# Kernel optimization log

Hardware: AMD Instinct MI355X
Metric: run time of the kernel (lower is better)

The kernel has to match this reference:

```python
import jax, jax.numpy as jnp
import numpy as np

# dims
L, E, D, DFF, H = 4, 4, 512, 2048, 8
B, T, S, K = 16, 256, 512, 2
HD = D // H


def _ln(x, g, b, eps=1e-5):
    m = x.mean(-1, keepdims=True)
    v = ((x - m) ** 2).mean(-1, keepdims=True)
    return (x - m) / jnp.sqrt(v + eps) * g + b


def _mha(xq, xkv, in_w, in_b, out_w, out_b):
    # torch nn.MultiheadAttention (batch_first), no masks, eval mode
    qw, kw, vw = jnp.split(in_w, 3, axis=0)
    qb, kb, vb = jnp.split(in_b, 3)
    q = xq @ qw.T + qb                       # [B,T,D]
    k = xkv @ kw.T + kb                      # [B,S,D]
    v = xkv @ vw.T + vb
    def heads(t):
        b, s, _ = t.shape
        return t.reshape(b, s, H, HD).transpose(0, 2, 1, 3)
    q, k, v = heads(q), heads(k), heads(v)   # [B,H,*,HD]
    scale = 1.0 / float(np.sqrt(HD))
    a = jax.nn.softmax(jnp.einsum('bhtd,bhsd->bhts', q, k) * scale, axis=-1)
    o = jnp.einsum('bhts,bhsd->bhtd', a, v)
    o = o.transpose(0, 2, 1, 3).reshape(xq.shape[0], xq.shape[1], D)
    return o @ out_w.T + out_b


def _expert(p, x, mem):
    (siw, sib, sow, sob, ciw, cib, cow, cob,
     l1w, l1b, l2w, l2b, g1, b1, g2, b2, g3, b3) = p
    sa = _mha(x, x, siw, sib, sow, sob)
    x = _ln(x + sa, g1, b1)
    ca = _mha(x, mem, ciw, cib, cow, cob)
    x = _ln(x + ca, g2, b2)
    ffn = jax.nn.relu(x @ l1w.T + l1b) @ l2w.T + l2b
    x = _ln(x + ffn, g3, b3)
    return x


def _forward(tgt, memory, router_w, params):
    x = tgt
    for l in range(L):
        pooled = x.mean(axis=1)                      # [B,D] sample-level routing
        logits = pooled @ router_w[l].T              # [B,E]
        vals, idx = jax.lax.top_k(logits, K)
        w = jax.nn.softmax(vals.astype(jnp.float32), axis=-1).astype(x.dtype)
        # dense [B,E] combine weights: zero for unselected experts -> same math
        wf = jnp.zeros((x.shape[0], E), x.dtype).at[jnp.arange(x.shape[0])[:, None], idx].add(w)
        p_l = jax.tree_util.tree_map(lambda a: a[l], params)   # each [E,...]
        outs = jax.vmap(_expert, in_axes=(0, None, None))(p_l, x, memory)  # [E,B,T,D]
        x = jnp.einsum('be,ebtd->btd', wf, outs)
    return x


def setup_inputs() -> dict:
    key = jax.random.key(0)
    ks = jax.random.split(key, 16)
    n = lambda k, shape: jax.random.normal(k, shape, jnp.float32) * 0.02
    return {
        'tgt': jax.random.normal(ks[0], (B, T, D), jnp.float32),
        'memory': jax.random.normal(ks[1], (B, S, D), jnp.float32),
        'router_w': n(ks[2], (L, E, D)),
        'sa_in_w': n(ks[3], (L, E, 3 * D, D)), 'sa_in_b': jnp.zeros((L, E, 3 * D)),
        'sa_out_w': n(ks[4], (L, E, D, D)), 'sa_out_b': jnp.zeros((L, E, D)),
        'ca_in_w': n(ks[5], (L, E, 3 * D, D)), 'ca_in_b': jnp.zeros((L, E, 3 * D)),
        'ca_out_w': n(ks[6], (L, E, D, D)), 'ca_out_b': jnp.zeros((L, E, D)),
        'lin1_w': n(ks[7], (L, E, DFF, D)), 'lin1_b': jnp.zeros((L, E, DFF)),
        'lin2_w': n(ks[8], (L, E, D, DFF)), 'lin2_b': jnp.zeros((L, E, D)),
        'n1_g': jnp.ones((L, E, D)), 'n1_b': jnp.zeros((L, E, D)),
        'n2_g': jnp.ones((L, E, D)), 'n2_b': jnp.zeros((L, E, D)),
        'n3_g': jnp.ones((L, E, D)), 'n3_b': jnp.zeros((L, E, D)),
    }


def reference(tgt, memory, router_w, sa_in_w, sa_in_b, sa_out_w, sa_out_b,
              ca_in_w, ca_in_b, ca_out_w, ca_out_b, lin1_w, lin1_b, lin2_w, lin2_b,
              n1_g, n1_b, n2_g, n2_b, n3_g, n3_b):
    params = (sa_in_w, sa_in_b, sa_out_w, sa_out_b, ca_in_w, ca_in_b, ca_out_w, ca_out_b,
              lin1_w, lin1_b, lin2_w, lin2_b, n1_g, n1_b, n2_g, n2_b, n3_g, n3_b)
    return _forward(tgt, memory, router_w, params)
```

## Files before the change

### kernel.cpp

```cpp
#include <hip/hip_runtime.h>
#include <hip/hip_bf16.h>

#define L_ 4
#define E_ 4
#define D_ 512
#define DFF_ 2048
#define H_ 8
#define B_ 16
#define T_ 256
#define S_ 512
#define HD_ 64
#define NSLOT 32

typedef __attribute__((ext_vector_type(4))) float f32x4;
typedef __attribute__((ext_vector_type(8))) short bf16x8;
typedef __attribute__((ext_vector_type(4))) int i32x4;

static __device__ __forceinline__ float bf2f(unsigned short u){
  union{float f; unsigned u;} c; c.u = ((unsigned)u)<<16; return c.f;
}
static __device__ __forceinline__ unsigned short f2bf(float f){
  union{float f; unsigned u;} c; c.f=f;
  unsigned u=c.u;
  return (unsigned short)((u + 0x7FFFu + ((u>>16)&1u))>>16);
}

static __device__ __forceinline__ void gload16(const unsigned short* g, unsigned short* l){
  __builtin_amdgcn_global_load_lds(
      (const __attribute__((address_space(1))) void*)g,
      (__attribute__((address_space(3))) void*)l, 16, 0, 0);
}

static __device__ __forceinline__ int xcd_swz(int orig, int nwg){
  int q = nwg >> 3, r = nwg & 7;
  int xcd = orig & 7, idx = orig >> 3;
  return (xcd < r) ? (xcd*(q+1) + idx) : (r*(q+1) + (xcd-r)*q + idx);
}

__global__ void __launch_bounds__(256) route_k(const float* __restrict__ x,
    const float* __restrict__ rw, int* __restrict__ eidx, float* __restrict__ wgt)
{
  __shared__ float pooled[D_];
  __shared__ float logit[E_];
  int b = blockIdx.x, tid = threadIdx.x;
  for (int d = tid; d < D_; d += 256) {
    float s = 0.f;
    const float* xp = x + ((long)b*T_)*D_ + d;
    for (int t=0;t<T_;t++) s += xp[(long)t*D_];
    pooled[d] = s * (1.f/T_);
  }
  __syncthreads();
  int wave = tid>>6, lane = tid&63;
  {
    float s=0.f;
    const float* w = rw + (long)wave*D_;
    for (int d=lane; d<D_; d+=64) s += pooled[d]*w[d];
    #pragma unroll
    for (int o=32;o;o>>=1) s += __shfl_xor(s,o);
    if (lane==0) logit[wave] = s;
  }
  __syncthreads();
  if (tid==0){
    int i1=0; float v1=logit[0];
    for (int e=1;e<E_;e++) if (logit[e] > v1){ v1=logit[e]; i1=e; }
    int i2=-1; float v2=-3.4e38f;
    for (int e=0;e<E_;e++) if (e!=i1 && logit[e] > v2){ v2=logit[e]; i2=e; }
    float e2 = __expf(v2 - v1);
    float w1 = 1.f/(1.f+e2);
    eidx[2*b]=i1; eidx[2*b+1]=i2;
    wgt[2*b]=w1; wgt[2*b+1]=e2*w1;
  }
}

__global__ void __launch_bounds__(256) cast_bf16_k(const float* __restrict__ in,
    unsigned short* __restrict__ out, long n){
  long i = ((long)blockIdx.x*blockDim.x + threadIdx.x)*4;
  long st = (long)gridDim.x*blockDim.x*4;
  for (; i<n; i+=st){
    float4 v = *(const float4*)(in+i);
    ushort4 o; o.x=f2bf(v.x); o.y=f2bf(v.y); o.z=f2bf(v.z); o.w=f2bf(v.w);
    *(ushort4*)(out+i) = o;
  }
}

__global__ void __launch_bounds__(256) cast_weights_k(
    const float* __restrict__ s0, const float* __restrict__ s1,
    const float* __restrict__ s2, const float* __restrict__ s3,
    const float* __restrict__ s4, const float* __restrict__ s5,
    unsigned short* __restrict__ d0, unsigned short* __restrict__ d1,
    unsigned short* __restrict__ d2, unsigned short* __restrict__ d3,
    unsigned short* __restrict__ d4, unsigned short* __restrict__ d5)
{
  const long N0=(long)E_*3*D_*D_, N1=(long)E_*D_*D_;
  const long N2=N0, N3=N1, N4=(long)E_*DFF_*D_, N5=N4;
  const long total = N0+N1+N2+N3+N4+N5;
  long i = ((long)blockIdx.x*256 + threadIdx.x)*4;
  long st = (long)gridDim.x*256*4;
  for (; i<total; i+=st){
    const float* s; unsigned short* d; long j = i;
    if (j < N0){ s=s0; d=d0; }
    else if ((j-=N0) < N1){ s=s1; d=d1; }
    else if ((j-=N1) < N2){ s=s2; d=d2; }
    else if ((j-=N2) < N3){ s=s3; d=d3; }
    else if ((j-=N3) < N4){ s=s4; d=d4; }
    else { j-=N4; s=s5; d=d5; }
    float4 v = *(const float4*)(s+j);
    ushort4 o; o.x=f2bf(v.x); o.y=f2bf(v.y); o.z=f2bf(v.z); o.w=f2bf(v.w);
    *(ushort4*)(d+j) = o;
  }
}

__global__ void __launch_bounds__(256) vtrans_k(const unsigned short* __restrict__ src,
    long sSlot, int ld, unsigned short* __restrict__ dst, int rows)
{
  __shared__ unsigned short t[64][68];
  int s0 = blockIdx.x*64; int h = blockIdx.y; int slot = blockIdx.z;
  const unsigned short* sp = src + (long)slot*sSlot + (long)h*64;
  int c = threadIdx.x&63, w = threadIdx.x>>6;
  #pragma unroll
  for (int i=0;i<16;i++){
    int r = i*4 + w;
    t[r][c] = sp[(long)(s0+r)*ld + c];
  }
  __syncthreads();
  unsigned short* dp = dst + ((long)slot*H_ + h)*((long)64*rows) + s0;
  #pragma unroll
  for (int i=0;i<16;i++){
    int d = i*4 + w;
    dp[(long)d*rows + c] = t[c][d];
  }
}

template<int NT>
__global__ void __launch_bounds__(256) fattn_k(
    const unsigned short* __restrict__ Qg, long qSlot, int ldq,
    const unsigned short* __restrict__ Kg, long kSlot, int ldk,
    const unsigned short* __restrict__ Vtg,
    unsigned short* __restrict__ Og, long oSlot, int ldo)
{
  constexpr int SLEN = NT*64;
  __shared__ unsigned short K_lds[64][72];
  __shared__ unsigned short V_lds[64][72];
  __shared__ unsigned short P_lds[4][16][72];

  int nwg = gridDim.x*gridDim.y;
  int wg = xcd_swz(blockIdx.x + gridDim.x*blockIdx.y, nwg);
  int qb = wg % gridDim.x;
  int z  = wg / gridDim.x;
  int slot = z >> 3, h = z & 7;
  int tid = threadIdx.x, wave = tid>>6, lane = tid&63;
  int lr = lane&15, lg = lane>>4;
  int lk = lg*8;

  const unsigned short* Qp = Qg + (long)slot*qSlot + (long)h*HD_;
  const unsigned short* Kp = Kg + (long)slot*kSlot + (long)h*HD_;
  const unsigned short* Vp = Vtg + (long)z*((long)HD_*SLEN);

  bf16x8 qf[2];
  {
    int qrow = qb*64 + wave*16 + lr;
    const unsigned short* qr = Qp + (long)qrow*ldq;
    qf[0] = *(const bf16x8*)(qr + lk);
    qf[1] = *(const bf16x8*)(qr + 32 + lk);
  }

  float m_prev[4], l_run[4];
  f32x4 acc_o[4];
  #pragma unroll
  for (int r=0;r<4;r++){ m_prev[r]=-1e30f; l_run[r]=0.f; }
  #pragma unroll
  for (int ni=0;ni<4;ni++) acc_o[ni]=(f32x4){0.f,0.f,0.f,0.f};

  int srow = tid>>3, sch = tid&7;

  i32x4 kr0 = *(const i32x4*)(Kp + (long)srow*ldk + sch*8);
  i32x4 kr1 = *(const i32x4*)(Kp + (long)(srow+32)*ldk + sch*8);
  i32x4 vr0 = *(const i32x4*)(Vp + (long)srow*SLEN + sch*8);
  i32x4 vr1 = *(const i32x4*)(Vp + (long)(srow+32)*SLEN + sch*8);

  for (int t=0; t<NT; ++t){
    __syncthreads();
    *(i32x4*)&K_lds[srow][sch*8] = kr0;
    *(i32x4*)&K_lds[srow+32][sch*8] = kr1;
    *(i32x4*)&V_lds[srow][sch*8] = vr0;
    *(i32x4*)&V_lds[srow+32][sch*8] = vr1;
    __syncthreads();

    int tn = (t+1 < NT) ? t+1 : t;
    int k0n = tn*64;
    kr0 = *(const i32x4*)(Kp + (long)(k0n+srow)*ldk + sch*8);
    kr1 = *(const i32x4*)(Kp + (long)(k0n+srow+32)*ldk + sch*8);
    vr0 = *(const i32x4*)(Vp + (long)srow*SLEN + k0n + sch*8);
    vr1 = *(const i32x4*)(Vp + (long)(srow+32)*SLEN + k0n + sch*8);

    f32x4 s[4];
    #pragma unroll
    for (int ni=0;ni<4;ni++) s[ni]=(f32x4){0.f,0.f,0.f,0.f};
    __builtin_amdgcn_s_setprio(1);
    #pragma unroll
    for (int ki=0;ki<2;ki++){
      #pragma unroll
      for (int ni=0;ni<4;ni++){
        bf16x8 kf = *(const bf16x8*)&K_lds[ni*16+lr][ki*32+lk];
        s[ni] = __builtin_amdgcn_mfma_f32_16x16x32_bf16(qf[ki], kf, s[ni],0,0,0);
      }
    }
    __builtin_amdgcn_s_setprio(0);
    float tmax[4], corr[4], mnew[4];
    #pragma unroll
    for (int r=0;r<4;r++){
      tmax[r] = fmaxf(fmaxf(s[0][r],s[1][r]),fmaxf(s[2][r],s[3][r]));
      #pragma unroll
      for (int msk=1; msk<16; msk<<=1) tmax[r]=fmaxf(tmax[r], __shfl_xor(tmax[r],msk));
      mnew[r] = fmaxf(m_prev[r], tmax[r]);
      corr[r] = __expf(m_prev[r]-mnew[r]);
      m_prev[r] = mnew[r];
    }
    float rs[4] = {0.f,0.f,0.f,0.f};
    #pragma unroll
    for (int ni=0;ni<4;ni++){
      #pragma unroll
      for (int r=0;r<4;r++){
        float p = __expf(s[ni][r]-mnew[r]);
        rs[r] += p;
        P_lds[wave][lg*4+r][ni*16+lr] = f2bf(p);
      }
    }
    #pragma unroll
    for (int r=0;r<4;r++){
      #pragma unroll
      for (int msk=1; msk<16; msk<<=1) rs[r] += __shfl_xor(rs[r],msk);
      l_run[r] = l_run[r]*corr[r] + rs[r];
      #pragma unroll
      for (int ni=0;ni<4;ni++) acc_o[ni][r] *= corr[r];
    }
    __builtin_amdgcn_s_setprio(1);
    #pragma unroll
    for (int ki=0;ki<2;ki++){
      bf16x8 pf = *(const bf16x8*)&P_lds[wave][lr][ki*32+lk];
      #pragma unroll
      for (int ni=0;ni<4;ni++){
        bf16x8 vf = *(const bf16x8*)&V_lds[ni*16+lr][ki*32+lk];
        acc_o[ni] = __builtin_amdgcn_mfma_f32_16x16x32_bf16(pf, vf, acc_o[ni],0,0,0);
      }
    }
    __builtin_amdgcn_s_setprio(0);
  }
  unsigned short* Op = Og + (long)slot*oSlot + (long)h*HD_;
  #pragma unroll
  for (int r=0;r<4;r++){
    float inv = 1.f/l_run[r];
    int q = qb*64 + wave*16 + lg*4 + r;
    #pragma unroll
    for (int ni=0;ni<4;ni++)
      Op[(long)q*ldo + ni*16 + lr] = f2bf(acc_o[ni][r]*inv);
  }
}

template<int BM, int BN, int WTM, int WTN, int BK>
__global__ void __launch_bounds__(512) gemm_lds(
    const unsigned short* __restrict__ A, long aSlot, int aDiv, long aHead, int lda,
    const unsigned short* __restrict__ W, long wSlot, long wHead, long wExp, int ldw,
    const int* __restrict__ eidx, const float* __restrict__ bias, long biasExp,
    void* __restrict__ Cp, long cSlot, long cHead, int ldc,
    int K, int HZ, int f32out, int relu, int scaleNlim, float scaleVal)
{
  constexpr int WAVES_N = BN/WTN;
  constexpr int MI = WTM/16, NI = WTN/16;
  constexpr int SLOTS = BK/8;
  static_assert((BM/WTM)*(BN/WTN) == 8, "8 waves");
  static_assert((BM*SLOTS)%512==0 && (BN*SLOTS)%512==0, "stage coverage");
  __shared__ unsigned short smem[2*(BM+BN)*BK];

  int nwg = gridDim.x*gridDim.y*gridDim.z;
  int wg = xcd_swz(blockIdx.x + gridDim.x*(blockIdx.y + gridDim.y*blockIdx.z), nwg);
  int bx = wg % gridDim.x; int t1 = wg / gridDim.x;
  int by = t1 % gridDim.y; int z  = t1 / gridDim.y;

  int slot = z / HZ;
  int h = z - slot*HZ;
  int e = eidx ? eidx[slot] : 0;
  const unsigned short* Ap = A + (long)(slot/aDiv)*aSlot + (long)h*aHead;
  const unsigned short* Wp = W + (long)slot*wSlot + (long)h*wHead + (long)e*wExp;
  const float* bp = bias ? (bias + (long)e*biasExp) : nullptr;

  int tid  = threadIdx.x;
  int wave = tid>>6, lane = tid&63;
  int wm = wave / WAVES_N, wn = wave % WAVES_N;
  int bm0 = by*BM;
  int bn0 = bx*BN;
  int lr = lane&15;
  int lg = lane>>4;
  int swz = (BK==64) ? (lr&7) : ((lr>>1)&3);

  Ap += (long)bm0*lda;
  Wp += (long)bn0*ldw;

  f32x4 acc[MI][NI];
  #pragma unroll
  for (int i=0;i<MI;i++)
  #pragma unroll
  for (int j=0;j<NI;j++) acc[i][j] = (f32x4){0.f,0.f,0.f,0.f};

  auto stage = [&](int buf, int k0){
    unsigned short* as = &smem[(size_t)buf*(BM+BN)*BK];
    unsigned short* bs = as + BM*BK;
    #pragma unroll
    for (int i=0;i<BM*SLOTS/512;i++){
      int cch = i*512 + tid;
      int row = cch / SLOTS, c = cch % SLOTS;
      int cs = (BK==64) ? (c ^ (row&7)) : (c ^ ((row>>1)&3));
      gload16(Ap + (long)row*lda + k0 + (cs<<3), as + cch*8);
    }
    #pragma unroll
    for (int i=0;i<BN*SLOTS/512;i++){
      int cch = i*512 + tid;
      int row = cch / SLOTS, c = cch % SLOTS;
      int cs = (BK==64) ? (c ^ (row&7)) : (c ^ ((row>>1)&3));
      gload16(Wp + (long)row*ldw + k0 + (cs<<3), bs + cch*8);
    }
  };

  auto compute = [&](int buf){
    unsigned short* as = &smem[(size_t)buf*(BM+BN)*BK];
    unsigned short* bs = as + BM*BK;
    #pragma unroll
    for (int ki=0;ki<BK/32;ki++){
      bf16x8 af[MI], bfr[NI];
      #pragma unroll
      for (int mi=0;mi<MI;mi++){
        int row = wm*WTM + mi*16 + lr;
        af[mi] = *(const bf16x8*)&as[row*BK + (((ki*4+lg) ^ swz)<<3)];
      }
      #pragma unroll
      for (int ni=0;ni<NI;ni++){
        int row = wn*WTN + ni*16 + lr;
        bfr[ni] = *(const bf16x8*)&bs[row*BK + (((ki*4+lg) ^ swz)<<3)];
      }
      __builtin_amdgcn_s_setprio(1);
      #pragma unroll
      for (int mi=0;mi<MI;mi++)
      #pragma unroll
      for (int ni=0;ni<NI;ni++)
        acc[mi][ni] = __builtin_amdgcn_mfma_f32_16x16x32_bf16(af[mi], bfr[ni], acc[mi][ni], 0,0,0);
      __builtin_amdgcn_s_setprio(0);
    }
  };

  int NT = K / BK;
  stage(0, 0);
  __syncthreads();
  int cur = 0;
  for (int t=0; t<NT; ++t){
    if (t+1 < NT) stage(cur^1, (t+1)*BK);
    compute(cur);
    __syncthreads();
    cur ^= 1;
  }

  long cbase = (long)slot*cSlot + (long)h*cHead;
  int rbase = lg*4;
  #pragma unroll
  for (int mi=0;mi<MI;mi++)
  #pragma unroll
  for (int ni=0;ni<NI;ni++){
    f32x4 v = acc[mi][ni];
    int n = bn0 + wn*WTN + ni*16 + lr;
    float bv = bp ? bp[n] : 0.f;
    float scv = (n < scaleNlim) ? scaleVal : 1.f;
    #pragma unroll
    for (int r=0;r<4;r++){
      int m = bm0 + wm*WTM + mi*16 + rbase + r;
      float val = (v[r] + bv) * scv;
      if (relu) val = fmaxf(val, 0.f);
      long o = cbase + (long)m*ldc + n;
      if (f32out) ((float*)Cp)[o] = val;
      else ((unsigned short*)Cp)[o] = f2bf(val);
    }
  }
}

__global__ void __launch_bounds__(256) add_ln_k(
    const float* __restrict__ Ab, int aDiv, long aStride,
    const float* __restrict__ Bb, long bStride,
    const float* __restrict__ G, const float* __restrict__ Bt,
    const int* __restrict__ eidx,
    float* __restrict__ OutF, unsigned short* __restrict__ OutB)
{
  int row = blockIdx.x*4 + (threadIdx.x>>6);
  int slot = row>>8, t = row&255;
  int lane = threadIdx.x&63;
  const float* a = Ab + (long)(slot/aDiv)*aStride + (long)t*D_;
  const float* b = Bb + (long)slot*bStride + (long)t*D_;
  int e = eidx[slot];
  const float* g  = G  + (long)e*D_;
  const float* bt = Bt + (long)e*D_;
  float x[8]; float s=0.f;
  #pragma unroll
  for (int i=0;i<8;i++){ x[i] = a[lane+i*64]+b[lane+i*64]; s+=x[i]; }
  #pragma unroll
  for (int o=32;o;o>>=1) s += __shfl_xor(s,o);
  float m = s*(1.f/D_);
  float q=0.f;
  #pragma unroll
  for (int i=0;i<8;i++){ float d=x[i]-m; q+=d*d; }
  #pragma unroll
  for (int o=32;o;o>>=1) q += __shfl_xor(q,o);
  float rs = rsqrtf(q*(1.f/D_)+1e-5f);
  long ob = (long)slot*(T_*D_) + (long)t*D_;
  #pragma unroll
  for (int i=0;i<8;i++){
    int d = lane+i*64;
    float y = (x[i]-m)*rs*g[d]+bt[d];
    OutF[ob+d]=y;
    if (OutB) OutB[ob+d]=f2bf(y);
  }
}

__global__ void __launch_bounds__(256) add_ln_comb_k(
    const float* __restrict__ x2, const float* __restrict__ proj,
    const float* __restrict__ G, const float* __restrict__ Bt,
    const int* __restrict__ eidx, const float* __restrict__ wgt,
    float* __restrict__ dstF, unsigned short* __restrict__ dstB)
{
  int row = blockIdx.x*4 + (threadIdx.x>>6);
  int b = row>>8, t = row&255;
  int lane = threadIdx.x&63;
  float out[8];
  #pragma unroll
  for (int i=0;i<8;i++) out[i]=0.f;
  #pragma unroll
  for (int s2i=0;s2i<2;s2i++){
    int slot = 2*b + s2i;
    int e = eidx[slot];
    float w = wgt[slot];
    const float* a = x2 + (long)slot*(T_*D_) + (long)t*D_;
    const float* p = proj + (long)slot*(T_*D_) + (long)t*D_;
    const float* g  = G  + (long)e*D_;
    const float* bt = Bt + (long)e*D_;
    float x[8]; float s=0.f;
    #pragma unroll
    for (int i=0;i<8;i++){ x[i] = a[lane+i*64]+p[lane+i*64]; s+=x[i]; }
    #pragma unroll
    for (int o=32;o;o>>=1) s += __shfl_xor(s,o);
    float m = s*(1.f/D_);
    float q=0.f;
    #pragma unroll
    for (int i=0;i<8;i++){ float d=x[i]-m; q+=d*d; }
    #pragma unroll
    for (int o=32;o;o>>=1) q += __shfl_xor(q,o);
    float rs = rsqrtf(q*(1.f/D_)+1e-5f);
    #pragma unroll
    for (int i=0;i<8;i++){
      int d = lane+i*64;
      out[i] += w*((x[i]-m)*rs*g[d]+bt[d]);
    }
  }
  long ob = (long)row*D_;
  #pragma unroll
  for (int i=0;i<8;i++){
    int d = lane+i*64;
    dstF[ob+d] = out[i];
    dstB[ob+d] = f2bf(out[i]);
  }
}

extern "C" void kernel_launch(void* const* d_in, const int* in_sizes, int n_in,
                              void* d_out, int out_size, void* d_ws, size_t ws_size,
                              hipStream_t stream)
{
  const float* tgt      = (const float*)d_in[0];
  const float* memory   = (const float*)d_in[1];
  const float* router_w = (const float*)d_in[2];
  const float* sa_in_w  = (const float*)d_in[3];
  const float* sa_in_b  = (const float*)d_in[4];
  const float* sa_out_w = (const float*)d_in[5];
  const float* sa_out_b = (const float*)d_in[6];
  const float* ca_in_w  = (const float*)d_in[7];
  const float* ca_in_b  = (const float*)d_in[8];
  const float* ca_out_w = (const float*)d_in[9];
  const float* ca_out_b = (const float*)d_in[10];
  const float* lin1_w   = (const float*)d_in[11];
  const float* lin1_b   = (const float*)d_in[12];
  const float* lin2_w   = (const float*)d_in[13];
  const float* lin2_b   = (const float*)d_in[14];
  const float* n1_g = (const float*)d_in[15];
  const float* n1_b = (const float*)d_in[16];
  const float* n2_g = (const float*)d_in[17];
  const float* n2_b = (const float*)d_in[18];
  const float* n3_g = (const float*)d_in[19];
  const float* n3_b = (const float*)d_in[20];

  char* ws = (char*)d_ws;
  size_t off = 0;
  auto alloc = [&](size_t bytes)->char*{
    char* p = ws + off; off += (bytes + 255) & ~(size_t)255; return p;
  };
  unsigned short* xb    = (unsigned short*)alloc(2ull*B_*T_*D_);
  unsigned short* memb  = (unsigned short*)alloc(2ull*B_*S_*D_);
  float*          x     = (float*)alloc(4ull*B_*T_*D_);
  int*            eidx  = (int*)alloc(4ull*NSLOT);
  float*          wgt   = (float*)alloc(4ull*NSLOT);
  unsigned short* wSaIn  = (unsigned short*)alloc(2ull*E_*3*D_*D_);
  unsigned short* wSaOut = (unsigned short*)alloc(2ull*E_*D_*D_);
  unsigned short* wCaIn  = (unsigned short*)alloc(2ull*E_*3*D_*D_);
  unsigned short* wCaOut = (unsigned short*)alloc(2ull*E_*D_*D_);
  unsigned short* wL1    = (unsigned short*)alloc(2ull*E_*DFF_*D_);
  unsigned short* wL2    = (unsigned short*)alloc(2ull*E_*D_*DFF_);
  unsigned short* qkv   = (unsigned short*)alloc(2ull*NSLOT*T_*3*D_);
  unsigned short* ffh   = (unsigned short*)alloc(2ull*NSLOT*T_*DFF_);
  unsigned short* attn  = (unsigned short*)alloc(2ull*NSLOT*T_*D_);
  float*          proj  = (float*)alloc(4ull*NSLOT*T_*D_);
  float*          x1    = (float*)alloc(4ull*NSLOT*T_*D_);
  unsigned short* x1b   = (unsigned short*)alloc(2ull*NSLOT*T_*D_);
  unsigned short* cq    = (unsigned short*)alloc(2ull*NSLOT*T_*D_);
  unsigned short* mkv   = (unsigned short*)alloc(2ull*NSLOT*S_*2*D_);
  float*          x2    = (float*)alloc(4ull*NSLOT*T_*D_);
  unsigned short* x2b   = (unsigned short*)alloc(2ull*NSLOT*T_*D_);
  unsigned short* Vt1   = cq;
  unsigned short* Vt2   = qkv;

  cast_bf16_k<<<1024,256,0,stream>>>(tgt,    xb,   (long)B_*T_*D_);
  cast_bf16_k<<<1024,256,0,stream>>>(memory, memb, (long)B_*S_*D_);

  const float* xcur = tgt;
  for (int l=0; l<L_; ++l){
    route_k<<<B_,256,0,stream>>>(xcur, router_w + (size_t)l*E_*D_, eidx, wgt);
    cast_weights_k<<<2048,256,0,stream>>>(
      sa_in_w  + (size_t)l*E_*3*D_*D_, sa_out_w + (size_t)l*E_*D_*D_,
      ca_in_w  + (size_t)l*E_*3*D_*D_, ca_out_w + (size_t)l*E_*D_*D_,
      lin1_w   + (size_t)l*E_*DFF_*D_, lin2_w   + (size_t)l*E_*D_*DFF_,
      wSaIn, wSaOut, wCaIn, wCaOut, wL1, wL2);

    gemm_lds<128,256,64,64,32><<<dim3(6,2,NSLOT),512,0,stream>>>(
      xb, (long)T_*D_, 2, 0, D_,
      wSaIn, 0, 0, (long)3*D_*D_, D_,
      eidx, sa_in_b + (size_t)l*E_*3*D_, 3*D_,
      qkv, (long)T_*3*D_, 0, 3*D_,
      512, 1, 0, 0, D_, 0.125f);
    vtrans_k<<<dim3(T_/64,H_,NSLOT),256,0,stream>>>(
      qkv + 2*D_, (long)T_*3*D_, 3*D_, Vt1, T_);
    fattn_k<4><<<dim3(T_/64, NSLOT*H_),256,0,stream>>>(
      qkv, (long)T_*3*D_, 3*D_,
      qkv + D_, (long)T_*3*D_, 3*D_,
      Vt1, attn, (long)T_*D_, D_);
    gemm_lds<128,128,64,32,64><<<dim3(4,2,NSLOT),512,0,stream>>>(
      attn, (long)T_*D_, 1, 0, D_,
      wSaOut, 0, 0, (long)D_*D_, D_,
      eidx, sa_out_b + (size_t)l*E_*D_, D_,
      proj, (long)T_*D_, 0, D_,
      512, 1, 1, 0, 0, 1.f);
    add_ln_k<<<2048,256,0,stream>>>(xcur, 2, (long)T_*D_, proj, (long)T_*D_,
      n1_g + (size_t)l*E_*D_, n1_b + (size_t)l*E_*D_, eidx, x1, x1b);
    gemm_lds<128,128,64,32,64><<<dim3(4,2,NSLOT),512,0,stream>>>(
      x1b, (long)T_*D_, 1, 0, D_,
      wCaIn, 0, 0, (long)3*D_*D_, D_,
      eidx, ca_in_b + (size_t)l*E_*3*D_, 3*D_,
      cq, (long)T_*D_, 0, D_,
      512, 1, 0, 0, D_, 0.125f);
    gemm_lds<128,256,64,64,32><<<dim3(4,4,NSLOT),512,0,stream>>>(
      memb, (long)S_*D_, 2, 0, D_,
      wCaIn + (size_t)D_*D_, 0, 0, (long)3*D_*D_, D_,
      eidx, ca_in_b + (size_t)l*E_*3*D_ + D_, 3*D_,
      mkv, (long)S_*2*D_, 0, 2*D_,
      512, 1, 0, 0, 0, 1.f);
    vtrans_k<<<dim3(S_/64,H_,NSLOT),256,0,stream>>>(
      mkv + D_, (long)S_*2*D_, 2*D_, Vt2, S_);
    fattn_k<8><<<dim3(T_/64, NSLOT*H_),256,0,stream>>>(
      cq, (long)T_*D_, D_,
      mkv, (long)S_*2*D_, 2*D_,
      Vt2, attn, (long)T_*D_, D_);
    gemm_lds<128,128,64,32,64><<<dim3(4,2,NSLOT),512,0,stream>>>(
      attn, (long)T_*D_, 1, 0, D_,
      wCaOut, 0, 0, (long)D_*D_, D_,
      eidx, ca_out_b + (size_t)l*E_*D_, D_,
      proj, (long)T_*D_, 0, D_,
      512, 1, 1, 0, 0, 1.f);
    add_ln_k<<<2048,256,0,stream>>>(x1, 1, (long)T_*D_, proj, (long)T_*D_,
      n2_g + (size_t)l*E_*D_, n2_b + (size_t)l*E_*D_, eidx, x2, x2b);
    gemm_lds<128,256,64,64,32><<<dim3(8,2,NSLOT),512,0,stream>>>(
      x2b, (long)T_*D_, 1, 0, D_,
      wL1, 0, 0, (long)DFF_*D_, D_,
      eidx, lin1_b + (size_t)l*E_*DFF_, DFF_,
      ffh, (long)T_*DFF_, 0, DFF_,
      512, 1, 0, 1, 0, 1.f);
    gemm_lds<128,128,64,32,64><<<dim3(4,2,NSLOT),512,0,stream>>>(
      ffh, (long)T_*DFF_, 1, 0, DFF_,
      wL2, 0, 0, (long)D_*DFF_, DFF_,
      eidx, lin2_b + (size_t)l*E_*D_, D_,
      proj, (long)T_*D_, 0, D_,
      2048, 1, 1, 0, 0, 1.f);
    float* dstF = (l==L_-1) ? (float*)d_out : x;
    add_ln_comb_k<<<1024,256,0,stream>>>(x2, proj,
      n3_g + (size_t)l*E_*D_, n3_b + (size_t)l*E_*D_, eidx, wgt, dstF, xb);
    xcur = x;
  }
}
```

Measured before the change: 1.093 ms.

## Split-K the D-output GEMMs into two partials and skip redundant softmax rescaling

The three GEMMs that produce D-wide fp32 outputs (self-attn out, cross-attn out, FFN lin2) are split along K into two halves. Each half writes to a separate buffer (proj, proj2), and the following add+LayerNorm kernels sum the two partials, so grids with few workgroups get twice as many. The flash-attention loop also skips the running-max correction (an exp plus rescaling of the accumulators) when no row max increases in the wave. The cost is an extra fp32 partial buffer write and read per GEMM, plus a divergent branch.

```diff
diff --git a/kernel.cpp b/kernel.cpp
--- a/kernel.cpp
+++ b/kernel.cpp
@@ -206,22 +206,31 @@
       }
     }
     __builtin_amdgcn_s_setprio(0);
-    float tmax[4], corr[4], mnew[4];
+    float tmax[4];
     #pragma unroll
     for (int r=0;r<4;r++){
       tmax[r] = fmaxf(fmaxf(s[0][r],s[1][r]),fmaxf(s[2][r],s[3][r]));
       #pragma unroll
       for (int msk=1; msk<16; msk<<=1) tmax[r]=fmaxf(tmax[r], __shfl_xor(tmax[r],msk));
-      mnew[r] = fmaxf(m_prev[r], tmax[r]);
-      corr[r] = __expf(m_prev[r]-mnew[r]);
-      m_prev[r] = mnew[r];
+    }
+    bool inc = (tmax[0]>m_prev[0])|(tmax[1]>m_prev[1])|(tmax[2]>m_prev[2])|(tmax[3]>m_prev[3]);
+    if (__any(inc)){
+      #pragma unroll
+      for (int r=0;r<4;r++){
+        float mnew = fmaxf(m_prev[r], tmax[r]);
+        float corr = __expf(m_prev[r]-mnew);
+        m_prev[r] = mnew;
+        l_run[r] *= corr;
+        #pragma unroll
+        for (int ni=0;ni<4;ni++) acc_o[ni][r] *= corr;
+      }
     }
     float rs[4] = {0.f,0.f,0.f,0.f};
     #pragma unroll
     for (int ni=0;ni<4;ni++){
       #pragma unroll
       for (int r=0;r<4;r++){
-        float p = __expf(s[ni][r]-mnew[r]);
+        float p = __expf(s[ni][r]-m_prev[r]);
         rs[r] += p;
         P_lds[wave][lg*4+r][ni*16+lr] = f2bf(p);
       }
@@ -230,9 +239,7 @@
     for (int r=0;r<4;r++){
       #pragma unroll
       for (int msk=1; msk<16; msk<<=1) rs[r] += __shfl_xor(rs[r],msk);
-      l_run[r] = l_run[r]*corr[r] + rs[r];
-      #pragma unroll
-      for (int ni=0;ni<4;ni++) acc_o[ni][r] *= corr[r];
+      l_run[r] += rs[r];
     }
     __builtin_amdgcn_s_setprio(1);
     #pragma unroll
@@ -257,12 +264,12 @@
   }
 }
 
-template<int BM, int BN, int WTM, int WTN, int BK>
+template<int BM, int BN, int WTM, int WTN, int BK, int KS>
 __global__ void __launch_bounds__(512) gemm_lds(
     const unsigned short* __restrict__ A, long aSlot, int aDiv, long aHead, int lda,
     const unsigned short* __restrict__ W, long wSlot, long wHead, long wExp, int ldw,
     const int* __restrict__ eidx, const float* __restrict__ bias, long biasExp,
-    void* __restrict__ Cp, long cSlot, long cHead, int ldc,
+    void* __restrict__ Cp, long cSlot, long cHead, int ldc, long cSplit,
     int K, int HZ, int f32out, int relu, int scaleNlim, float scaleVal)
 {
   constexpr int WAVES_N = BN/WTN;
@@ -275,14 +282,15 @@
   int nwg = gridDim.x*gridDim.y*gridDim.z;
   int wg = xcd_swz(blockIdx.x + gridDim.x*(blockIdx.y + gridDim.y*blockIdx.z), nwg);
   int bx = wg % gridDim.x; int t1 = wg / gridDim.x;
-  int by = t1 % gridDim.y; int z  = t1 / gridDim.y;
-
+  int by = t1 % gridDim.y; int zz = t1 / gridDim.y;
+
+  int ks = zz % KS; int z = zz / KS;
   int slot = z / HZ;
   int h = z - slot*HZ;
   int e = eidx ? eidx[slot] : 0;
-  const unsigned short* Ap = A + (long)(slot/aDiv)*aSlot + (long)h*aHead;
-  const unsigned short* Wp = W + (long)slot*wSlot + (long)h*wHead + (long)e*wExp;
-  const float* bp = bias ? (bias + (long)e*biasExp) : nullptr;
+  const unsigned short* Ap = A + (long)(slot/aDiv)*aSlot + (long)h*aHead + (long)ks*K;
+  const unsigned short* Wp = W + (long)slot*wSlot + (long)h*wHead + (long)e*wExp + (long)ks*K;
+  const float* bp = (bias && ks==0) ? (bias + (long)e*biasExp) : nullptr;
 
   int tid  = threadIdx.x;
   int wave = tid>>6, lane = tid&63;
@@ -358,7 +366,7 @@
     cur ^= 1;
   }
 
-  long cbase = (long)slot*cSlot + (long)h*cHead;
+  long cbase = (long)slot*cSlot + (long)h*cHead + (long)ks*cSplit;
   int rbase = lg*4;
   #pragma unroll
   for (int mi=0;mi<MI;mi++)
@@ -382,7 +390,7 @@
 
 __global__ void __launch_bounds__(256) add_ln_k(
     const float* __restrict__ Ab, int aDiv, long aStride,
-    const float* __restrict__ Bb, long bStride,
+    const float* __restrict__ Bb, const float* __restrict__ Bb2, long bStride,
     const float* __restrict__ G, const float* __restrict__ Bt,
     const int* __restrict__ eidx,
     float* __restrict__ OutF, unsigned short* __restrict__ OutB)
@@ -392,12 +400,17 @@
   int lane = threadIdx.x&63;
   const float* a = Ab + (long)(slot/aDiv)*aStride + (long)t*D_;
   const float* b = Bb + (long)slot*bStride + (long)t*D_;
+  const float* b2 = Bb2 ? (Bb2 + (long)slot*bStride + (long)t*D_) : nullptr;
   int e = eidx[slot];
   const float* g  = G  + (long)e*D_;
   const float* bt = Bt + (long)e*D_;
   float x[8]; float s=0.f;
   #pragma unroll
-  for (int i=0;i<8;i++){ x[i] = a[lane+i*64]+b[lane+i*64]; s+=x[i]; }
+  for (int i=0;i<8;i++){
+    float v = a[lane+i*64]+b[lane+i*64];
+    if (b2) v += b2[lane+i*64];
+    x[i]=v; s+=v;
+  }
   #pragma unroll
   for (int o=32;o;o>>=1) s += __shfl_xor(s,o);
   float m = s*(1.f/D_);
@@ -418,7 +431,7 @@
 }
 
 __global__ void __launch_bounds__(256) add_ln_comb_k(
-    const float* __restrict__ x2, const float* __restrict__ proj,
+    const float* __restrict__ x2, const float* __restrict__ proj, const float* __restrict__ proj2,
     const float* __restrict__ G, const float* __restrict__ Bt,
     const int* __restrict__ eidx, const float* __restrict__ wgt,
     float* __restrict__ dstF, unsigned short* __restrict__ dstB)
@@ -436,11 +449,12 @@
     float w = wgt[slot];
     const float* a = x2 + (long)slot*(T_*D_) + (long)t*D_;
     const float* p = proj + (long)slot*(T_*D_) + (long)t*D_;
+    const float* p2 = proj2 + (long)slot*(T_*D_) + (long)t*D_;
     const float* g  = G  + (long)e*D_;
     const float* bt = Bt + (long)e*D_;
     float x[8]; float s=0.f;
     #pragma unroll
-    for (int i=0;i<8;i++){ x[i] = a[lane+i*64]+p[lane+i*64]; s+=x[i]; }
+    for (int i=0;i<8;i++){ x[i] = a[lane+i*64]+p[lane+i*64]+p2[lane+i*64]; s+=x[i]; }
     #pragma unroll
     for (int o=32;o;o>>=1) s += __shfl_xor(s,o);
     float m = s*(1.f/D_);
@@ -511,6 +525,7 @@
   unsigned short* ffh   = (unsigned short*)alloc(2ull*NSLOT*T_*DFF_);
   unsigned short* attn  = (unsigned short*)alloc(2ull*NSLOT*T_*D_);
   float*          proj  = (float*)alloc(4ull*NSLOT*T_*D_);
+  float*          proj2 = (float*)alloc(4ull*NSLOT*T_*D_);
   float*          x1    = (float*)alloc(4ull*NSLOT*T_*D_);
   unsigned short* x1b   = (unsigned short*)alloc(2ull*NSLOT*T_*D_);
   unsigned short* cq    = (unsigned short*)alloc(2ull*NSLOT*T_*D_);
@@ -519,6 +534,7 @@
   unsigned short* x2b   = (unsigned short*)alloc(2ull*NSLOT*T_*D_);
   unsigned short* Vt1   = cq;
   unsigned short* Vt2   = qkv;
+  long projSplit = (long)(proj2 - proj);
 
   cast_bf16_k<<<1024,256,0,stream>>>(tgt,    xb,   (long)B_*T_*D_);
   cast_bf16_k<<<1024,256,0,stream>>>(memory, memb, (long)B_*S_*D_);
@@ -532,11 +548,11 @@
       lin1_w   + (size_t)l*E_*DFF_*D_, lin2_w   + (size_t)l*E_*D_*DFF_,
       wSaIn, wSaOut, wCaIn, wCaOut, wL1, wL2);
 
-    gemm_lds<128,256,64,64,32><<<dim3(6,2,NSLOT),512,0,stream>>>(
+    gemm_lds<128,256,64,64,32,1><<<dim3(6,2,NSLOT),512,0,stream>>>(
       xb, (long)T_*D_, 2, 0, D_,
       wSaIn, 0, 0, (long)3*D_*D_, D_,
       eidx, sa_in_b + (size_t)l*E_*3*D_, 3*D_,
-      qkv, (long)T_*3*D_, 0, 3*D_,
+      qkv, (long)T_*3*D_, 0, 3*D_, 0,
       512, 1, 0, 0, D_, 0.125f);
     vtrans_k<<<dim3(T_/64,H_,NSLOT),256,0,stream>>>(
       qkv + 2*D_, (long)T_*3*D_, 3*D_, Vt1, T_);
@@ -544,25 +560,25 @@
       qkv, (long)T_*3*D_, 3*D_,
       qkv + D_, (long)T_*3*D_, 3*D_,
       Vt1, attn, (long)T_*D_, D_);
-    gemm_lds<128,128,64,32,64><<<dim3(4,2,NSLOT),512,0,stream>>>(
+    gemm_lds<128,128,64,32,64,2><<<dim3(4,2,NSLOT*2),512,0,stream>>>(
       attn, (long)T_*D_, 1, 0, D_,
       wSaOut, 0, 0, (long)D_*D_, D_,
       eidx, sa_out_b + (size_t)l*E_*D_, D_,
-      proj, (long)T_*D_, 0, D_,
-      512, 1, 1, 0, 0, 1.f);
-    add_ln_k<<<2048,256,0,stream>>>(xcur, 2, (long)T_*D_, proj, (long)T_*D_,
+      proj, (long)T_*D_, 0, D_, projSplit,
+      256, 1, 1, 0, 0, 1.f);
+    add_ln_k<<<2048,256,0,stream>>>(xcur, 2, (long)T_*D_, proj, proj2, (long)T_*D_,
       n1_g + (size_t)l*E_*D_, n1_b + (size_t)l*E_*D_, eidx, x1, x1b);
-    gemm_lds<128,128,64,32,64><<<dim3(4,2,NSLOT),512,0,stream>>>(
+    gemm_lds<128,128,64,32,64,1><<<dim3(4,2,NSLOT),512,0,stream>>>(
       x1b, (long)T_*D_, 1, 0, D_,
       wCaIn, 0, 0, (long)3*D_*D_, D_,
       eidx, ca_in_b + (size_t)l*E_*3*D_, 3*D_,
-      cq, (long)T_*D_, 0, D_,
+      cq, (long)T_*D_, 0, D_, 0,
       512, 1, 0, 0, D_, 0.125f);
-    gemm_lds<128,256,64,64,32><<<dim3(4,4,NSLOT),512,0,stream>>>(
+    gemm_lds<128,256,64,64,32,1><<<dim3(4,4,NSLOT),512,0,stream>>>(
       memb, (long)S_*D_, 2, 0, D_,
       wCaIn + (size_t)D_*D_, 0, 0, (long)3*D_*D_, D_,
       eidx, ca_in_b + (size_t)l*E_*3*D_ + D_, 3*D_,
-      mkv, (long)S_*2*D_, 0, 2*D_,
+      mkv, (long)S_*2*D_, 0, 2*D_, 0,
       512, 1, 0, 0, 0, 1.f);
     vtrans_k<<<dim3(S_/64,H_,NSLOT),256,0,stream>>>(
       mkv + D_, (long)S_*2*D_, 2*D_, Vt2, S_);
@@ -570,28 +586,28 @@
       cq, (long)T_*D_, D_,
       mkv, (long)S_*2*D_, 2*D_,
       Vt2, attn, (long)T_*D_, D_);
-    gemm_lds<128,128,64,32,64><<<dim3(4,2,NSLOT),512,0,stream>>>(
+    gemm_lds<128,128,64,32,64,2><<<dim3(4,2,NSLOT*2),512,0,stream>>>(
       attn, (long)T_*D_, 1, 0, D_,
       wCaOut, 0, 0, (long)D_*D_, D_,
       eidx, ca_out_b + (size_t)l*E_*D_, D_,
-      proj, (long)T_*D_, 0, D_,
-      512, 1, 1, 0, 0, 1.f);
-    add_ln_k<<<2048,256,0,stream>>>(x1, 1, (long)T_*D_, proj, (long)T_*D_,
+      proj, (long)T_*D_, 0, D_, projSplit,
+      256, 1, 1, 0, 0, 1.f);
+    add_ln_k<<<2048,256,0,stream>>>(x1, 1, (long)T_*D_, proj, proj2, (long)T_*D_,
       n2_g + (size_t)l*E_*D_, n2_b + (size_t)l*E_*D_, eidx, x2, x2b);
-    gemm_lds<128,256,64,64,32><<<dim3(8,2,NSLOT),512,0,stream>>>(
+    gemm_lds<128,256,64,64,32,1><<<dim3(8,2,NSLOT),512,0,stream>>>(
       x2b, (long)T_*D_, 1, 0, D_,
       wL1, 0, 0, (long)DFF_*D_, D_,
       eidx, lin1_b + (size_t)l*E_*DFF_, DFF_,
-      ffh, (long)T_*DFF_, 0, DFF_,
+      ffh, (long)T_*DFF_, 0, DFF_, 0,
       512, 1, 0, 1, 0, 1.f);
-    gemm_lds<128,128,64,32,64><<<dim3(4,2,NSLOT),512,0,stream>>>(
+    gemm_lds<128,128,64,32,64,2><<<dim3(4,2,NSLOT*2),512,0,stream>>>(
       ffh, (long)T_*DFF_, 1, 0, DFF_,
       wL2, 0, 0, (long)D_*DFF_, DFF_,
       eidx, lin2_b + (size_t)l*E_*D_, D_,
-      proj, (long)T_*D_, 0, D_,
-      2048, 1, 1, 0, 0, 1.f);
+      proj, (long)T_*D_, 0, D_, projSplit,
+      1024, 1, 1, 0, 0, 1.f);
     float* dstF = (l==L_-1) ? (float*)d_out : x;
-    add_ln_comb_k<<<1024,256,0,stream>>>(x2, proj,
+    add_ln_comb_k<<<1024,256,0,stream>>>(x2, proj, proj2,
       n3_g + (size_t)l*E_*D_, n3_b + (size_t)l*E_*D_, eidx, wgt, dstF, xb);
     xcur = x;
   }
```

New measurement: 1.135 ms. 1.04x slower.
